# Kernel tuning notes

Hardware: AMD Instinct MI355X
Metric: run time of the kernel (lower is better)

The kernel has to match this reference:

```python
import jax, jax.numpy as jnp
import numpy as np

LN_EPS = 1e-5
L1_EPS = 1e-12  # F.normalize clamp_min eps


def _layernorm(h, g, b):
    mu = h.mean(-1, keepdims=True)
    var = ((h - mu) ** 2).mean(-1, keepdims=True)
    return (h - mu) * jax.lax.rsqrt(var + LN_EPS) * g + b


def _graph(x, wq_w, wq_b, wk_w, wk_b, gcn_w, ln_g, ln_b):
    # x: [..., n, d]
    qx = x @ wq_w.T + wq_b
    kx = x @ wk_w.T + wk_b
    dot = jnp.einsum('...nd,...md->...nm', qx, kx)
    sq = dot * dot
    adj = sq / jnp.maximum(sq.sum(-1, keepdims=True), L1_EPS)  # L1-normalized rows
    for i in range(gcn_w.shape[0]):
        h = adj @ (x @ gcn_w[i])
        x = jax.nn.relu(_layernorm(h, ln_g[i], ln_b[i]))
    return x.mean(-2)  # mean over nodes -> [..., d]


def setup_inputs() -> dict:
    key = jax.random.key(0)
    ks = jax.random.split(key, 12)
    N, FR, B, NF = 16, 32, 50, 768
    L, NC = 2, 400
    s = 1.0 / np.sqrt(NF)
    inp = {
        'feats': jax.random.normal(ks[0], (N, FR, B, NF), jnp.float32),
        'feat_global_single': jax.random.normal(ks[1], (N, NF), jnp.float32),
        'feat_single_previous': jax.random.normal(ks[2], (N, NF), jnp.float32),
        'wq_w': jax.random.normal(ks[3], (NF, NF), jnp.float32) * s,
        'wq_b': jnp.zeros((NF,), jnp.float32),
        'wk_w': jax.random.normal(ks[4], (NF, NF), jnp.float32) * s,
        'wk_b': jnp.zeros((NF,), jnp.float32),
        'gcn_w': jax.random.normal(ks[5], (L, NF, NF), jnp.float32) * s,
        'ln_g': jnp.ones((L, NF), jnp.float32),
        'ln_b': jnp.zeros((L, NF), jnp.float32),
        'fc1_w': jax.random.normal(ks[6], (NF, 2 * NF), jnp.float32) / np.sqrt(2 * NF),
        'fc1_b': jnp.zeros((NF,), jnp.float32),
        'fc2_w': jax.random.normal(ks[7], (NC, NF), jnp.float32) * s,
        'fc2_b': jnp.zeros((NC,), jnp.float32),
        't_c': 0,
    }
    return inp


def reference(feats, feat_global_single, feat_single_previous,
              wq_w, wq_b, wk_w, wk_b, gcn_w, ln_g, ln_b,
              fc1_w, fc1_b, fc2_w, fc2_b, t_c):
    N, FR, B, NF = feats.shape
    x = feats.reshape(N * FR, B, NF)
    # object-level graph (shared weights)
    x = _graph(x, wq_w, wq_b, wk_w, wk_b, gcn_w, ln_g, ln_b)  # [N*FR, NF]
    x = x.reshape(N, FR, NF)
    # frame-level graph (same shared weights)
    x = _graph(x, wq_w, wq_b, wk_w, wk_b, gcn_w, ln_g, ln_b)  # [N, NF]
    y = jnp.concatenate([x, feat_global_single], axis=-1)      # [N, 2*NF]
    # ClassifierSimple (dropout = identity in eval)
    h = jax.nn.relu(y @ fc1_w.T + fc1_b)
    logits = h @ fc2_w.T + fc2_b
    return (logits, y)
```

## Files before the change

kernel.cpp:

```cpp
#include <hip/hip_runtime.h>
#include <hip/hip_bf16.h>

typedef unsigned short u16;
typedef unsigned int   u32;
typedef __attribute__((ext_vector_type(8))) short short8;
typedef __attribute__((ext_vector_type(4))) float float4v;

__device__ __forceinline__ float bf2f(u16 u){ union{u32 i; float f;} c; c.i = ((u32)u) << 16; return c.f; }
__device__ __forceinline__ float bflo(u32 u){ union{u32 i; float f;} c; c.i = u << 16; return c.f; }
__device__ __forceinline__ float bfhi(u32 u){ union{u32 i; float f;} c; c.i = u & 0xFFFF0000u; return c.f; }
__device__ __forceinline__ u16 f2bf(float f){
  union{float f; u32 i;} c; c.f = f; u32 x = c.i;
  return (u16)((x + 0x7FFFu + ((x >> 16) & 1u)) >> 16);
}
__device__ __forceinline__ u32 pack2(float a, float b){
  union { __hip_bfloat162 h; u32 u; } c;
  c.h = __float22bfloat162_rn(float2{a, b});
  return c.u;
}

__device__ __forceinline__ void async16(const void* g, void* l){
  __builtin_amdgcn_global_load_lds((const __attribute__((address_space(1))) void*)g,
                                   (__attribute__((address_space(3))) void*)l, 16, 0, 0);
}

__global__ void prep_w(const float* __restrict__ wq, const float* __restrict__ wk,
                       const float* __restrict__ gcn,
                       u16* __restrict__ WqT, u16* __restrict__ WkT,
                       u16* __restrict__ QHB768, u16* __restrict__ gcnT1)
{
  __shared__ float tile[32][33];
  int z = blockIdx.z;
  const float* src = (z == 0) ? wq : (z == 1) ? wk : gcn + (size_t)(z - 2) * 589824;
  u16* dst = (z == 0) ? WqT : (z == 1) ? WkT : (z == 2) ? QHB768 : gcnT1;
  int r0 = blockIdx.y * 32, c0 = blockIdx.x * 32;
  int tx = threadIdx.x, ty = threadIdx.y;
  for (int i = 0; i < 32; i += 8) tile[ty + i][tx] = src[(size_t)(r0 + ty + i) * 768 + c0 + tx];
  __syncthreads();
  for (int i = 0; i < 32; i += 8) dst[(size_t)(c0 + ty + i) * 768 + r0 + tx] = f2bf(tile[tx][ty + i]);
}

__global__ void __launch_bounds__(256) prep_uv2(const float* __restrict__ wq, const float* __restrict__ wk,
                                                const float* __restrict__ wqb, const float* __restrict__ wkb,
                                                float* __restrict__ uv, float* __restrict__ cbuf)
{
  __shared__ float red[4][64];
  __shared__ float r2[256];
  int b = blockIdx.x, tid = threadIdx.x;
  if (b < 24) {
    const float* w  = (b < 12) ? wq : wk;
    const float* bs = (b < 12) ? wkb : wqb;
    int out = (b % 12) * 64 + (tid & 63);
    int oq = tid >> 6;
    float a = 0.f;
    for (int o = oq * 192; o < oq * 192 + 192; o++) a += w[(size_t)o * 768 + out] * bs[o];
    red[oq][tid & 63] = a;
    __syncthreads();
    if (tid < 64)
      uv[((b < 12) ? 0 : 768) + (b % 12) * 64 + tid] = red[0][tid] + red[1][tid] + red[2][tid] + red[3][tid];
  } else {
    float a = 0.f;
    for (int o = tid; o < 768; o += 256) a += wqb[o] * wkb[o];
    r2[tid] = a; __syncthreads();
    if (tid == 0) { float s = 0.f; for (int i = 0; i < 256; i++) s += r2[i]; cbuf[0] = s; }
  }
}

__global__ void __launch_bounds__(256) conv_pq(const float* __restrict__ src, u16* __restrict__ dst,
                                               const float* __restrict__ uv, const float* __restrict__ cbuf,
                                               float* __restrict__ p, float* __restrict__ q)
{
  __shared__ float us[768], vs[768];
  int tid = threadIdx.x, lane = tid & 63;
  for (int i = tid; i < 768; i += 256) { us[i] = uv[i]; vs[i] = uv[768 + i]; }
  __syncthreads();
  size_t rbase = (size_t)blockIdx.x * 8;
  int row = tid >> 5;
  int c3  = (tid & 31) * 3;
  const float* s = src + (rbase + row) * 768 + (size_t)c3 * 8;
  u16* d = dst + (rbase + row) * 768 + (size_t)c3 * 8;
  float ap = 0.f, aq = 0.f;
#pragma unroll
  for (int j = 0; j < 3; j++) {
    float4 a = ((const float4*)s)[j * 2];
    float4 b = ((const float4*)s)[j * 2 + 1];
    uint4 o = { pack2(a.x, a.y), pack2(a.z, a.w), pack2(b.x, b.y), pack2(b.z, b.w) };
    ((uint4*)d)[j] = o;
    const float* uu = &us[(c3 + j) * 8];
    const float* vv = &vs[(c3 + j) * 8];
    ap += a.x*uu[0] + a.y*uu[1] + a.z*uu[2] + a.w*uu[3] + b.x*uu[4] + b.y*uu[5] + b.z*uu[6] + b.w*uu[7];
    aq += a.x*vv[0] + a.y*vv[1] + a.z*vv[2] + a.w*vv[3] + b.x*vv[4] + b.y*vv[5] + b.z*vv[6] + b.w*vv[7];
  }
  for (int m = 1; m <= 16; m <<= 1) { ap += __shfl_xor(ap, m); aq += __shfl_xor(aq, m); }
  if ((lane & 31) == 0) {
    p[rbase + row] = ap + cbuf[0];
    q[rbase + row] = aq;
  }
}

__global__ void __launch_bounds__(256) gemm_bt(const u16* __restrict__ A, const u16* __restrict__ Bw,
                                               const float* __restrict__ bias, u16* __restrict__ C,
                                               int M, int N, int K, int ny0)
{
  __shared__ __attribute__((aligned(16))) u16 As[128 * 64];
  __shared__ __attribute__((aligned(16))) u16 Bs[128 * 64];
  int tid = threadIdx.x, lane = tid & 63, wid = tid >> 6;
  int wm = wid >> 1, wn = wid & 1;
  size_t m0 = (size_t)blockIdx.x * 128, n0 = (size_t)(blockIdx.y + ny0) * 128;

  float4v acc[4][4];
  for (int r = 0; r < 4; r++) for (int c = 0; c < 4; c++) acc[r][c] = (float4v){0.f, 0.f, 0.f, 0.f};

  int srow8  = lane >> 3;
  int schunk = (lane & 7) ^ srow8;
  const u16* gA[4]; const u16* gB[4];
  u16* lA[4]; u16* lB[4];
#pragma unroll
  for (int j = 0; j < 4; j++) {
    int r = 32 * wid + 8 * j + srow8;
    gA[j] = A  + (m0 + r) * (size_t)K + schunk * 8;
    gB[j] = Bw + (n0 + r) * (size_t)K + schunk * 8;
    lA[j] = &As[(32 * wid + 8 * j) * 64];
    lB[j] = &Bs[(32 * wid + 8 * j) * 64];
  }

  int l15 = lane & 15, quad = lane >> 4;
  int s0 = quad ^ (l15 & 7);

  for (int kt = 0; kt < K; kt += 64) {
#pragma unroll
    for (int j = 0; j < 4; j++) {
      async16(gA[j] + kt, lA[j]);
      async16(gB[j] + kt, lB[j]);
    }
    __syncthreads();
#pragma unroll
    for (int ks = 0; ks < 2; ks++) {
      int so = (s0 ^ (ks << 2)) * 8;
      short8 af[4], bfr[4];
#pragma unroll
      for (int r = 0; r < 4; r++) af[r]  = *(const short8*)&As[(wm * 64 + r * 16 + l15) * 64 + so];
#pragma unroll
      for (int c = 0; c < 4; c++) bfr[c] = *(const short8*)&Bs[(wn * 64 + c * 16 + l15) * 64 + so];
#pragma unroll
      for (int r = 0; r < 4; r++)
#pragma unroll
        for (int c = 0; c < 4; c++)
          acc[r][c] = __builtin_amdgcn_mfma_f32_16x16x32_bf16(af[r], bfr[c], acc[r][c], 0, 0, 0);
    }
    __syncthreads();
  }

  int quad4 = quad * 4;
  for (int c = 0; c < 4; c++) {
    int n = (int)n0 + wn * 64 + c * 16 + l15;
    float bv = bias ? bias[n] : 0.f;
    for (int r = 0; r < 4; r++) {
      size_t mbase = m0 + wm * 64 + r * 16 + quad4;
      for (int t = 0; t < 4; t++)
        C[(mbase + t) * (size_t)N + n] = f2bf(acc[r][c][t] + bv);
    }
  }
}


template<int NP>
__global__ void __launch_bounds__(512) fused_l1(const u16* __restrict__ TH, const u16* __restrict__ AR,
                                                const float* __restrict__ pb, const float* __restrict__ qb,
                                                const float* __restrict__ lng, const float* __restrict__ lnb,
                                                u16* __restrict__ adjG, u16* __restrict__ X, int n, int Mtot)
{
  constexpr int ST = 72;
  constexpr int TPW = (NP == 64) ? 2 : 1;
  __shared__ __attribute__((aligned(16))) u16 adjb[NP * ST];
  __shared__ __attribute__((aligned(16))) u16 HT[2][64 * ST];
  __shared__ __attribute__((aligned(16))) u16 As1[NP * 64];
  __shared__ __attribute__((aligned(16))) u16 Bs1[NP * 64];
  __shared__ float rsum[NP];
  __shared__ float stats[NP][2];
  __shared__ float bc[NP][2];
  __shared__ float ps[NP], qs[NP];
  __shared__ float lg[768], lb[768];

  int g = blockIdx.x;
  int tid = threadIdx.x, lane = tid & 63, w = tid >> 6;
  int l15 = lane & 15, quad = lane >> 4;

  for (int i = tid; i < 768; i += 512) { lg[i] = lng[i]; lb[i] = lnb[i]; }
  if (tid < NP) {
    rsum[tid] = 0.f; stats[tid][0] = 0.f; stats[tid][1] = 0.f;
    ps[tid] = (tid < n) ? pb[(size_t)g * n + tid] : 0.f;
    qs[tid] = (tid < n) ? qb[(size_t)g * n + tid] : 0.f;
  }
  __syncthreads();

  int mt, nt0; bool s_act;
  if (NP == 64) { mt = w & 3; nt0 = (w >> 2) * 2; s_act = true; }
  else          { mt = w & 1; nt0 = w >> 1;       s_act = (w < 4); }

  int srow8  = lane >> 3;
  int schunk = (lane & 7) ^ srow8;
  int trow   = (NP == 64) ? (8 * w + srow8) : (8 * (w & 3) + srow8);
  size_t grow = (size_t)g * n + trow;
  if (grow >= (size_t)Mtot) grow = Mtot - 1;
  const u16* gA1 = TH + grow * 1536 + schunk * 8;
  const u16* gB1 = AR + grow * 768  + schunk * 8;
  u16* lA1 = &As1[((NP == 64) ? 8 * w : 8 * (w & 3)) * 64];
  u16* lB1 = &Bs1[((NP == 64) ? 8 * w : 8 * (w & 3)) * 64];
  int s0 = quad ^ (l15 & 7);

  float4v sacc[TPW];
  for (int j = 0; j < TPW; j++) sacc[j] = (float4v){0.f, 0.f, 0.f, 0.f};

  for (int kt = 0; kt < 768; kt += 64) {
    if (NP == 64) {
      async16(gA1 + kt, lA1);
      async16(gB1 + kt, lB1);
    } else {
      if (w < 4) async16(gA1 + kt, lA1);
      else       async16(gB1 + kt, lB1);
    }
    __syncthreads();
    if (s_act) {
#pragma unroll
      for (int ks = 0; ks < 2; ks++) {
        int so = (s0 ^ (ks << 2)) * 8;
        short8 a = *(const short8*)&As1[(mt * 16 + l15) * 64 + so];
#pragma unroll
        for (int j = 0; j < TPW; j++) {
          short8 b = *(const short8*)&Bs1[((nt0 + j) * 16 + l15) * 64 + so];
          sacc[j] = __builtin_amdgcn_mfma_f32_16x16x32_bf16(a, b, sacc[j], 0, 0, 0);
        }
      }
    }
    __syncthreads();
  }

  if (s_act) {
    for (int j = 0; j < TPW; j++) {
      int col = (nt0 + j) * 16 + l15;
      bool cok = col < n;
      for (int t = 0; t < 4; t++) {
        int row = mt * 16 + quad * 4 + t;
        sacc[j][t] = cok ? (sacc[j][t] + ps[row] + qs[col]) : 0.f;
      }
    }
    for (int t = 0; t < 4; t++) {
      float s = 0.f;
      for (int j = 0; j < TPW; j++) { float v = sacc[j][t]; s += v * v; }
      s += __shfl_xor(s, 1); s += __shfl_xor(s, 2); s += __shfl_xor(s, 4); s += __shfl_xor(s, 8);
      if (l15 == 0) atomicAdd(&rsum[mt * 16 + quad * 4 + t], s);
    }
  }
  __syncthreads();
  if (tid < NP) rsum[tid] = 1.0f / fmaxf(rsum[tid], 1e-12f);
  __syncthreads();
  if (s_act) {
    u16* gadj = adjG + (size_t)g * NP * NP;
    for (int j = 0; j < TPW; j++)
      for (int t = 0; t < 4; t++) {
        int row = mt * 16 + quad * 4 + t, col = (nt0 + j) * 16 + l15;
        float v = sacc[j][t];
        u16 b = f2bf(v * v * rsum[row]);
        adjb[row * ST + col] = b;
        gadj[row * NP + col] = b;
      }
  }
  __syncthreads();

  int m2, nt20;
  if (NP == 64) { m2 = w & 3; nt20 = (w >> 2) * 2; }
  else          { m2 = w & 1; nt20 = w >> 1; }

  float4v xacc[12][TPW];
#pragma unroll
  for (int ch = 0; ch < 12; ch++) for (int j = 0; j < TPW; j++) xacc[ch][j] = (float4v){0.f,0.f,0.f,0.f};

  int hj  = tid & (NP - 1);
  int hseg= (NP == 64) ? w : ((tid >> 5) & 7);
  bool hact = (NP == 64) ? true : (tid < NP * 8);
  const u16* hbase = TH + ((size_t)g * n + hj) * 1536 + 768 + hseg * 8;

  uint4 hcur = {0,0,0,0};
  if (hact && hj < n) hcur = *(const uint4*)(hbase);

#pragma unroll
  for (int ch = 0; ch < 12; ch++) {
    uint4 hnext = {0,0,0,0};
    if (ch < 11 && hact && hj < n) hnext = *(const uint4*)(hbase + (ch + 1) * 64);
    u16* htb = HT[ch & 1];
    if (hact) {
      const u16* ep = (const u16*)&hcur;
      for (int i = 0; i < 8; i++) htb[(hseg * 8 + i) * ST + hj] = ep[i];
    }
    __syncthreads();
    for (int k = 0; k < NP / 32; k++) {
      short8 a = *(const short8*)&adjb[(m2 * 16 + l15) * ST + k * 32 + quad * 8];
      for (int j = 0; j < TPW; j++) {
        short8 b = *(const short8*)&htb[((nt20 + j) * 16 + l15) * ST + k * 32 + quad * 8];
        xacc[ch][j] = __builtin_amdgcn_mfma_f32_16x16x32_bf16(a, b, xacc[ch][j], 0, 0, 0);
      }
    }
    hcur = hnext;
  }

  float ssum[4] = {0,0,0,0}, ssq[4] = {0,0,0,0};
#pragma unroll
  for (int ch = 0; ch < 12; ch++)
    for (int j = 0; j < TPW; j++)
      for (int t = 0; t < 4; t++) { float v = xacc[ch][j][t]; ssum[t] += v; ssq[t] += v * v; }
  for (int m = 1; m <= 8; m <<= 1)
    for (int t = 0; t < 4; t++) { ssum[t] += __shfl_xor(ssum[t], m); ssq[t] += __shfl_xor(ssq[t], m); }
  if (l15 == 0)
    for (int t = 0; t < 4; t++) {
      atomicAdd(&stats[m2 * 16 + quad * 4 + t][0], ssum[t]);
      atomicAdd(&stats[m2 * 16 + quad * 4 + t][1], ssq[t]);
    }
  __syncthreads();
  if (tid < NP) {
    float mu = stats[tid][0] * (1.f / 768.f);
    float var = stats[tid][1] * (1.f / 768.f) - mu * mu;
    bc[tid][0] = mu; bc[tid][1] = rsqrtf(fmaxf(var, 0.f) + 1e-5f);
  }
  __syncthreads();

#pragma unroll
  for (int ch = 0; ch < 12; ch++)
    for (int j = 0; j < TPW; j++)
      for (int t = 0; t < 4; t++) {
        int row = m2 * 16 + quad * 4 + t;
        if (row < n) {
          int d = ch * 64 + (nt20 + j) * 16 + l15;
          float v = fmaxf((xacc[ch][j][t] - bc[row][0]) * bc[row][1] * lg[d] + lb[d], 0.f);
          X[((size_t)g * n + row) * 768 + d] = f2bf(v);
        }
      }
}

template<int NP>
__global__ void __launch_bounds__(512) fused_l2(const u16* __restrict__ adjG, const u16* __restrict__ H,
                                                const float* __restrict__ lng, const float* __restrict__ lnb,
                                                u16* __restrict__ Xmean, int n, float inv,
                                                const float* __restrict__ uvg, const float* __restrict__ cbuf,
                                                float* __restrict__ pOut, float* __restrict__ qOut)
{
  constexpr int ST = 72;
  constexpr int TPW = (NP == 64) ? 2 : 1;
  __shared__ __attribute__((aligned(16))) u16 adjb[NP * ST];
  __shared__ __attribute__((aligned(16))) u16 HT[2][64 * ST];
  __shared__ float stats[NP][2];
  __shared__ float bc[NP][2];
  __shared__ float colsum[768];
  __shared__ float lg[768], lb[768];
  __shared__ float pr[8][2];

  int g = blockIdx.x;
  int tid = threadIdx.x, lane = tid & 63, w = tid >> 6;
  int l15 = lane & 15, quad = lane >> 4;

  for (int i = tid; i < 768; i += 512) { lg[i] = lng[i]; lb[i] = lnb[i]; colsum[i] = 0.f; }
  if (tid < NP) { stats[tid][0] = 0.f; stats[tid][1] = 0.f; }
  if (tid * 8 < NP * NP) {
    int row = (tid * 8) / NP, c0 = (tid * 8) % NP;
    uint4 v = *(const uint4*)(adjG + (size_t)g * NP * NP + row * NP + c0);
    *(uint4*)&adjb[row * ST + c0] = v;
  }

  int m2, nt20;
  if (NP == 64) { m2 = w & 3; nt20 = (w >> 2) * 2; }
  else          { m2 = w & 1; nt20 = w >> 1; }

  float4v xacc[12][TPW];
#pragma unroll
  for (int ch = 0; ch < 12; ch++) for (int j = 0; j < TPW; j++) xacc[ch][j] = (float4v){0.f,0.f,0.f,0.f};

  int hj  = tid & (NP - 1);
  int hseg= (NP == 64) ? w : ((tid >> 5) & 7);
  bool hact = (NP == 64) ? true : (tid < NP * 8);
  const u16* hbase = H + ((size_t)g * n + hj) * 768 + hseg * 8;

  uint4 hcur = {0,0,0,0};
  if (hact && hj < n) hcur = *(const uint4*)(hbase);

  __syncthreads();

#pragma unroll
  for (int ch = 0; ch < 12; ch++) {
    uint4 hnext = {0,0,0,0};
    if (ch < 11 && hact && hj < n) hnext = *(const uint4*)(hbase + (ch + 1) * 64);
    u16* htb = HT[ch & 1];
    if (hact) {
      const u16* ep = (const u16*)&hcur;
      for (int i = 0; i < 8; i++) htb[(hseg * 8 + i) * ST + hj] = ep[i];
    }
    __syncthreads();
    for (int k = 0; k < NP / 32; k++) {
      short8 a = *(const short8*)&adjb[(m2 * 16 + l15) * ST + k * 32 + quad * 8];
      for (int j = 0; j < TPW; j++) {
        short8 b = *(const short8*)&htb[((nt20 + j) * 16 + l15) * ST + k * 32 + quad * 8];
        xacc[ch][j] = __builtin_amdgcn_mfma_f32_16x16x32_bf16(a, b, xacc[ch][j], 0, 0, 0);
      }
    }
    hcur = hnext;
  }

  float ssum[4] = {0,0,0,0}, ssq[4] = {0,0,0,0};
#pragma unroll
  for (int ch = 0; ch < 12; ch++)
    for (int j = 0; j < TPW; j++)
      for (int t = 0; t < 4; t++) { float v = xacc[ch][j][t]; ssum[t] += v; ssq[t] += v * v; }
  for (int m = 1; m <= 8; m <<= 1)
    for (int t = 0; t < 4; t++) { ssum[t] += __shfl_xor(ssum[t], m); ssq[t] += __shfl_xor(ssq[t], m); }
  if (l15 == 0)
    for (int t = 0; t < 4; t++) {
      atomicAdd(&stats[m2 * 16 + quad * 4 + t][0], ssum[t]);
      atomicAdd(&stats[m2 * 16 + quad * 4 + t][1], ssq[t]);
    }
  __syncthreads();
  if (tid < NP) {
    float mu = stats[tid][0] * (1.f / 768.f);
    float var = stats[tid][1] * (1.f / 768.f) - mu * mu;
    bc[tid][0] = mu; bc[tid][1] = rsqrtf(fmaxf(var, 0.f) + 1e-5f);
  }
  __syncthreads();

#pragma unroll
  for (int ch = 0; ch < 12; ch++)
    for (int j = 0; j < TPW; j++)
      for (int t = 0; t < 4; t++) {
        int row = m2 * 16 + quad * 4 + t;
        int d = ch * 64 + (nt20 + j) * 16 + l15;
        float v = fmaxf((xacc[ch][j][t] - bc[row][0]) * bc[row][1] * lg[d] + lb[d], 0.f);
        float vm = (row < n) ? v : 0.f;
        vm += __shfl_xor(vm, 16);
        vm += __shfl_xor(vm, 32);
        if (quad == 0) atomicAdd(&colsum[d], vm);
      }
  __syncthreads();
  if (tid < 384)
    ((u32*)Xmean)[(size_t)g * 384 + tid] = pack2(colsum[tid * 2] * inv, colsum[tid * 2 + 1] * inv);

  if (pOut) {
    float pp = 0.f, qq = 0.f;
    if (tid < 384) {
      float x0 = colsum[tid * 2] * inv, x1 = colsum[tid * 2 + 1] * inv;
      pp = x0 * uvg[tid * 2] + x1 * uvg[tid * 2 + 1];
      qq = x0 * uvg[768 + tid * 2] + x1 * uvg[768 + tid * 2 + 1];
    }
    for (int m = 1; m <= 32; m <<= 1) { pp += __shfl_xor(pp, m); qq += __shfl_xor(qq, m); }
    if (lane == 0) { pr[w][0] = pp; pr[w][1] = qq; }
    __syncthreads();
    if (tid == 0) {
      float sp = 0.f, sq = 0.f;
      for (int i = 0; i < 8; i++) { sp += pr[i][0]; sq += pr[i][1]; }
      pOut[g] = sp + cbuf[0]; qOut[g] = sq;
    }
  }
}

__global__ void __launch_bounds__(384) concat_y(const u16* __restrict__ Xm,
                                                const float* __restrict__ fgs, float* __restrict__ yout)
{
  int b = blockIdx.x, tid = threadIdx.x;
  u32 u = ((const u32*)Xm)[(size_t)b * 384 + tid];
  int d0 = tid * 2;
  yout[(size_t)b * 1536 + d0]     = bflo(u);
  yout[(size_t)b * 1536 + d0 + 1] = bfhi(u);
  yout[(size_t)b * 1536 + 768 + d0]     = fgs[(size_t)b * 768 + d0];
  yout[(size_t)b * 1536 + 768 + d0 + 1] = fgs[(size_t)b * 768 + d0 + 1];
}

__global__ void __launch_bounds__(256) fc1_relu(const float* __restrict__ yout,
                                                const float* __restrict__ fc1w, const float* __restrict__ fc1b,
                                                float* __restrict__ h)
{
  int o = blockIdx.x * 4 + (threadIdx.x >> 6);
  int lane = threadIdx.x & 63;
  float acc[16];
  for (int b = 0; b < 16; b++) acc[b] = 0.f;
  const float4* wr = (const float4*)(fc1w + (size_t)o * 1536);
  for (int k4 = lane; k4 < 384; k4 += 64) {
    float4 wv = wr[k4];
    for (int b = 0; b < 16; b++) {
      float4 yv = ((const float4*)(yout + (size_t)b * 1536))[k4];
      acc[b] += wv.x * yv.x + wv.y * yv.y + wv.z * yv.z + wv.w * yv.w;
    }
  }
  for (int m = 1; m <= 32; m <<= 1)
    for (int b = 0; b < 16; b++) acc[b] += __shfl_xor(acc[b], m);
  if (lane < 16) h[(size_t)lane * 768 + o] = fmaxf(acc[lane] + fc1b[o], 0.f);
}

__global__ void __launch_bounds__(256) fc2_out(const float* __restrict__ h,
                                               const float* __restrict__ fc2w, const float* __restrict__ fc2b,
                                               float* __restrict__ logits)
{
  int o = blockIdx.x * 4 + (threadIdx.x >> 6);
  int lane = threadIdx.x & 63;
  float acc[16];
  for (int b = 0; b < 16; b++) acc[b] = 0.f;
  const float4* wr = (const float4*)(fc2w + (size_t)o * 768);
  for (int k4 = lane; k4 < 192; k4 += 64) {
    float4 wv = wr[k4];
    for (int b = 0; b < 16; b++) {
      float4 hv = ((const float4*)(h + (size_t)b * 768))[k4];
      acc[b] += wv.x * hv.x + wv.y * hv.y + wv.z * hv.z + wv.w * hv.w;
    }
  }
  for (int m = 1; m <= 32; m <<= 1)
    for (int b = 0; b < 16; b++) acc[b] += __shfl_xor(acc[b], m);
  if (lane < 16) logits[(size_t)lane * 400 + o] = acc[lane] + fc2b[o];
}

extern "C" void kernel_launch(void* const* d_in, const int* in_sizes, int n_in,
                              void* d_out, int out_size, void* d_ws, size_t ws_size,
                              hipStream_t stream) {
  const float* feats = (const float*)d_in[0];
  const float* fgs   = (const float*)d_in[1];
  const float* wq_w  = (const float*)d_in[3];
  const float* wq_b  = (const float*)d_in[4];
  const float* wk_w  = (const float*)d_in[5];
  const float* wk_b  = (const float*)d_in[6];
  const float* gcn_w = (const float*)d_in[7];
  const float* ln_g  = (const float*)d_in[8];
  const float* ln_b  = (const float*)d_in[9];
  const float* fc1_w = (const float*)d_in[10];
  const float* fc1_b = (const float*)d_in[11];
  const float* fc2_w = (const float*)d_in[12];
  const float* fc2_b = (const float*)d_in[13];
  float* out  = (float*)d_out;
  float* yout = out + 16 * 400;

  char* ws = (char*)d_ws;
  size_t off = 0;
  auto alloc = [&](size_t b){ size_t r = off; off = (off + b + 255) & ~(size_t)255; return r; };
  u16*  QHB    = (u16*) (ws + alloc((size_t)1536 * 768 * 2));
  u16*  gcnT1  = (u16*) (ws + alloc((size_t)768 * 768 * 2));
  u16*  WqT    = (u16*) (ws + alloc((size_t)768 * 768 * 2));
  u16*  WkT    = (u16*) (ws + alloc((size_t)768 * 768 * 2));
  float* uv    = (float*)(ws + alloc((size_t)1536 * 4));
  float* cbuf  = (float*)(ws + alloc((size_t)4));
  u16*  Abf    = (u16*) (ws + alloc((size_t)25600 * 768 * 2));
  float* pObj  = (float*)(ws + alloc((size_t)25600 * 4));
  float* qObj  = (float*)(ws + alloc((size_t)25600 * 4));
  float* pF    = (float*)(ws + alloc((size_t)512 * 4));
  float* qF    = (float*)(ws + alloc((size_t)512 * 4));
  u16*  Xf     = (u16*) (ws + alloc((size_t)512 * 768 * 2));
  u16*  QHf    = (u16*) (ws + alloc((size_t)512 * 1536 * 2));
  u16*  X1f    = (u16*) (ws + alloc((size_t)512 * 768 * 2));
  u16*  H2f    = (u16*) (ws + alloc((size_t)512 * 768 * 2));
  u16*  adjFb  = (u16*) (ws + alloc((size_t)16 * 32 * 32 * 2));
  u16*  Xm     = (u16*) (ws + alloc((size_t)16 * 768 * 2));
  float* hbuf  = (float*)(ws + alloc((size_t)16 * 768 * 4));
  size_t base = off;

  auto need = [&](int GC){
    size_t R = (size_t)GC * 50;
    return base + R * 1536 * 2 + 512 + R * 768 * 2 + 512 + (size_t)GC * 64 * 64 * 2 + 512;
  };
  int GC = 64;
  if (need(512) <= ws_size) GC = 512;
  else if (need(256) <= ws_size) GC = 256;
  else if (need(128) <= ws_size) GC = 128;
  int R = GC * 50;
  size_t off2 = base;
  auto alloc2 = [&](size_t b){ size_t r = off2; off2 = (off2 + b + 255) & ~(size_t)255; return r; };
  u16* QHc   = (u16*)(ws + alloc2((size_t)R * 1536 * 2));
  u16* X1c   = (u16*)(ws + alloc2((size_t)R * 768 * 2));
  u16* adjGc = (u16*)(ws + alloc2((size_t)GC * 64 * 64 * 2));
  u16* H2c   = QHc;

  prep_w<<<dim3(24, 24, 4), dim3(32, 8), 0, stream>>>(wq_w, wk_w, gcn_w, WqT, WkT,
                                                      QHB + (size_t)768 * 768, gcnT1);
  prep_uv2<<<25, 256, 0, stream>>>(wq_w, wk_w, wq_b, wk_b, uv, cbuf);
  gemm_bt<<<dim3(6, 6), 256, 0, stream>>>(WkT, WqT, nullptr, QHB, 768, 768, 768, 0);
  conv_pq<<<3200, 256, 0, stream>>>(feats, Abf, uv, cbuf, pObj, qObj);

  int nchunks = 512 / GC;
  for (int c = 0; c < nchunks; c++) {
    const u16* fc = Abf + (size_t)c * GC * 50 * 768;
    gemm_bt<<<dim3(R / 128, 6), 256, 0, stream>>>(fc, QHB, nullptr, QHc, R, 1536, 768, 0);
    gemm_bt<<<dim3(R / 128, 6), 256, 0, stream>>>(fc, QHB, nullptr, QHc, R, 1536, 768, 6);
    fused_l1<64><<<GC, 512, 0, stream>>>(QHc, fc, pObj + (size_t)c * GC * 50, qObj + (size_t)c * GC * 50,
                                         ln_g, ln_b, adjGc, X1c, 50, R);
    gemm_bt<<<dim3(R / 128, 6), 256, 0, stream>>>(X1c, gcnT1, nullptr, H2c, R, 768, 768, 0);
    fused_l2<64><<<GC, 512, 0, stream>>>(adjGc, H2c, ln_g + 768, ln_b + 768,
                                         Xf + (size_t)c * GC * 768, 50, 1.f / 50.f,
                                         uv, cbuf, pF + (size_t)c * GC, qF + (size_t)c * GC);
  }

  gemm_bt<<<dim3(4, 12), 256, 0, stream>>>(Xf, QHB, nullptr, QHf, 512, 1536, 768, 0);
  fused_l1<32><<<16, 512, 0, stream>>>(QHf, Xf, pF, qF, ln_g, ln_b, adjFb, X1f, 32, 512);
  gemm_bt<<<dim3(4, 6), 256, 0, stream>>>(X1f, gcnT1, nullptr, H2f, 512, 768, 768, 0);
  fused_l2<32><<<16, 512, 0, stream>>>(adjFb, H2f, ln_g + 768, ln_b + 768, Xm, 32, 1.f / 32.f,
                                       uv, cbuf, nullptr, nullptr);

  concat_y<<<16, 384, 0, stream>>>(Xm, fgs, yout);
  fc1_relu<<<192, 256, 0, stream>>>(yout, fc1_w, fc1_b, hbuf);
  fc2_out<<<100, 256, 0, stream>>>(hbuf, fc2_w, fc2_b, out);
}
```

Measured before the change: 506.2 us.

## Prefetch all H chunks upfront and stage full H tile in LDS

```diff
diff --git a/kernel.cpp b/kernel.cpp
--- a/kernel.cpp
+++ b/kernel.cpp
@@ -173,7 +173,7 @@
   constexpr int ST = 72;
   constexpr int TPW = (NP == 64) ? 2 : 1;
   __shared__ __attribute__((aligned(16))) u16 adjb[NP * ST];
-  __shared__ __attribute__((aligned(16))) u16 HT[2][64 * ST];
+  __shared__ __attribute__((aligned(16))) u16 HT[12][64 * ST];
   __shared__ __attribute__((aligned(16))) u16 As1[NP * 64];
   __shared__ __attribute__((aligned(16))) u16 Bs1[NP * 64];
   __shared__ float rsum[NP];
@@ -185,6 +185,17 @@
   int g = blockIdx.x;
   int tid = threadIdx.x, lane = tid & 63, w = tid >> 6;
   int l15 = lane & 15, quad = lane >> 4;
+
+  int hj  = tid & (NP - 1);
+  int hseg= (NP == 64) ? w : ((tid >> 5) & 7);
+  bool hact = (NP == 64) ? true : (tid < NP * 8);
+  const u16* hbase = TH + ((size_t)g * n + hj) * 1536 + 768 + hseg * 8;
+  uint4 hv[12];
+#pragma unroll
+  for (int ch = 0; ch < 12; ch++) {
+    hv[ch] = (uint4){0, 0, 0, 0};
+    if (hact && hj < n) hv[ch] = *(const uint4*)(hbase + ch * 64);
+  }
 
   for (int i = tid; i < 768; i += 512) { lg[i] = lng[i]; lb[i] = lnb[i]; }
   if (tid < NP) {
@@ -266,7 +277,6 @@
         gadj[row * NP + col] = b;
       }
   }
-  __syncthreads();
 
   int m2, nt20;
   if (NP == 64) { m2 = w & 3; nt20 = (w >> 2) * 2; }
@@ -276,32 +286,24 @@
 #pragma unroll
   for (int ch = 0; ch < 12; ch++) for (int j = 0; j < TPW; j++) xacc[ch][j] = (float4v){0.f,0.f,0.f,0.f};
 
-  int hj  = tid & (NP - 1);
-  int hseg= (NP == 64) ? w : ((tid >> 5) & 7);
-  bool hact = (NP == 64) ? true : (tid < NP * 8);
-  const u16* hbase = TH + ((size_t)g * n + hj) * 1536 + 768 + hseg * 8;
-
-  uint4 hcur = {0,0,0,0};
-  if (hact && hj < n) hcur = *(const uint4*)(hbase);
-
 #pragma unroll
   for (int ch = 0; ch < 12; ch++) {
-    uint4 hnext = {0,0,0,0};
-    if (ch < 11 && hact && hj < n) hnext = *(const uint4*)(hbase + (ch + 1) * 64);
-    u16* htb = HT[ch & 1];
     if (hact) {
-      const u16* ep = (const u16*)&hcur;
-      for (int i = 0; i < 8; i++) htb[(hseg * 8 + i) * ST + hj] = ep[i];
-    }
-    __syncthreads();
+      const u16* ep = (const u16*)&hv[ch];
+      for (int i = 0; i < 8; i++) HT[ch][(hseg * 8 + i) * ST + hj] = ep[i];
+    }
+  }
+  __syncthreads();
+
+#pragma unroll
+  for (int ch = 0; ch < 12; ch++) {
     for (int k = 0; k < NP / 32; k++) {
       short8 a = *(const short8*)&adjb[(m2 * 16 + l15) * ST + k * 32 + quad * 8];
       for (int j = 0; j < TPW; j++) {
-        short8 b = *(const short8*)&htb[((nt20 + j) * 16 + l15) * ST + k * 32 + quad * 8];
+        short8 b = *(const short8*)&HT[ch][((nt20 + j) * 16 + l15) * ST + k * 32 + quad * 8];
         xacc[ch][j] = __builtin_amdgcn_mfma_f32_16x16x32_bf16(a, b, xacc[ch][j], 0, 0, 0);
       }
     }
-    hcur = hnext;
   }
 
   float ssum[4] = {0,0,0,0}, ssq[4] = {0,0,0,0};
@@ -347,7 +349,7 @@
   constexpr int ST = 72;
   constexpr int TPW = (NP == 64) ? 2 : 1;
   __shared__ __attribute__((aligned(16))) u16 adjb[NP * ST];
-  __shared__ __attribute__((aligned(16))) u16 HT[2][64 * ST];
+  __shared__ __attribute__((aligned(16))) u16 HT[12][64 * ST];
   __shared__ float stats[NP][2];
   __shared__ float bc[NP][2];
   __shared__ float colsum[768];
@@ -357,6 +359,17 @@
   int g = blockIdx.x;
   int tid = threadIdx.x, lane = tid & 63, w = tid >> 6;
   int l15 = lane & 15, quad = lane >> 4;
+
+  int hj  = tid & (NP - 1);
+  int hseg= (NP == 64) ? w : ((tid >> 5) & 7);
+  bool hact = (NP == 64) ? true : (tid < NP * 8);
+  const u16* hbase = H + ((size_t)g * n + hj) * 768 + hseg * 8;
+  uint4 hv[12];
+#pragma unroll
+  for (int ch = 0; ch < 12; ch++) {
+    hv[ch] = (uint4){0, 0, 0, 0};
+    if (hact && hj < n) hv[ch] = *(const uint4*)(hbase + ch * 64);
+  }
 
   for (int i = tid; i < 768; i += 512) { lg[i] = lng[i]; lb[i] = lnb[i]; colsum[i] = 0.f; }
   if (tid < NP) { stats[tid][0] = 0.f; stats[tid][1] = 0.f; }
@@ -374,34 +387,24 @@
 #pragma unroll
   for (int ch = 0; ch < 12; ch++) for (int j = 0; j < TPW; j++) xacc[ch][j] = (float4v){0.f,0.f,0.f,0.f};
 
-  int hj  = tid & (NP - 1);
-  int hseg= (NP == 64) ? w : ((tid >> 5) & 7);
-  bool hact = (NP == 64) ? true : (tid < NP * 8);
-  const u16* hbase = H + ((size_t)g * n + hj) * 768 + hseg * 8;
-
-  uint4 hcur = {0,0,0,0};
-  if (hact && hj < n) hcur = *(const uint4*)(hbase);
-
-  __syncthreads();
-
 #pragma unroll
   for (int ch = 0; ch < 12; ch++) {
-    uint4 hnext = {0,0,0,0};
-    if (ch < 11 && hact && hj < n) hnext = *(const uint4*)(hbase + (ch + 1) * 64);
-    u16* htb = HT[ch & 1];
     if (hact) {
-      const u16* ep = (const u16*)&hcur;
-      for (int i = 0; i < 8; i++) htb[(hseg * 8 + i) * ST + hj] = ep[i];
-    }
-    __syncthreads();
+      const u16* ep = (const u16*)&hv[ch];
+      for (int i = 0; i < 8; i++) HT[ch][(hseg * 8 + i) * ST + hj] = ep[i];
+    }
+  }
+  __syncthreads();
+
+#pragma unroll
+  for (int ch = 0; ch < 12; ch++) {
     for (int k = 0; k < NP / 32; k++) {
       short8 a = *(const short8*)&adjb[(m2 * 16 + l15) * ST + k * 32 + quad * 8];
       for (int j = 0; j < TPW; j++) {
-        short8 b = *(const short8*)&htb[((nt20 + j) * 16 + l15) * ST + k * 32 + quad * 8];
+        short8 b = *(const short8*)&HT[ch][((nt20 + j) * 16 + l15) * ST + k * 32 + quad * 8];
         xacc[ch][j] = __builtin_amdgcn_mfma_f32_16x16x32_bf16(a, b, xacc[ch][j], 0, 0, 0);
       }
     }
-    hcur = hnext;
   }
 
   float ssum[4] = {0,0,0,0}, ssq[4] = {0,0,0,0};
```

Measured after the change: 524.8 us. 1.04x slower.
